# Optimization experiments

Measured on AMD Instinct MI355X. Metric: run time of the kernel, lower is better.

Reference implementation:

```python
import jax, jax.numpy as jnp
import numpy as np

N, D, F, C = 50000, 32, 128, 16
LN_EPS = 1e-5
CLAMP_MIN = 1e-5


def _layernorm_1d(x):
    # LayerNorm over the full node vector, no affine (elementwise_affine=False)
    m = x.mean()
    v = x.var()  # biased, matches torch LayerNorm
    return (x - m) / jnp.sqrt(v + LN_EPS)


def setup_inputs() -> dict:
    key = jax.random.key(0)
    k1, k2, k3, k4, k5, k6 = jax.random.split(key, 6)
    return {
        "h": jax.random.normal(k1, (N, F), dtype=jnp.float32),
        "logits": jax.random.normal(k2, (N, C), dtype=jnp.float32),
        "old_z": jax.random.uniform(k3, (N,), dtype=jnp.float32),
        "tau_1": jax.random.uniform(k4, (1,), dtype=jnp.float32),
        "tau_2": jax.random.uniform(k5, (1,), dtype=jnp.float32),
        "nbr": jax.random.randint(k6, (N, D), 0, N, dtype=jnp.int32),
    }


def reference(h, logits, old_z, tau_1, tau_2, nbr):
    # --- mailbox pass 1: neighbor logits -> adaptive gating features ---
    pred = jnp.argmax(logits[nbr], axis=2)          # [N, D] neighbor class preds
    center_pred = jnp.argmax(logits, axis=1)        # [N]
    # n_degree = 1 in the source (counts, not fractions) -- reproduced faithfully
    f1 = jnp.sum(pred == center_pred[:, None], axis=1).astype(h.dtype)  # [N]
    cnts = jax.nn.one_hot(pred, C, dtype=h.dtype).sum(axis=1)           # [N, C]
    cnts_p = jnp.clip(cnts, CLAMP_MIN, None)
    f2 = -jnp.sum(cnts_p * jnp.log(cnts_p), axis=1)                     # [N]
    f1 = jax.lax.stop_gradient(f1)
    f2 = jax.lax.stop_gradient(f2)

    norm_f1 = _layernorm_1d(f1)
    norm_f2 = _layernorm_1d(f2)
    # shared_tau=True path: tau_1, tau_2 passed in ([1] broadcasts over [N])
    z = jax.nn.sigmoid(-(norm_f1 - tau_1)) * jax.nn.sigmoid(-(norm_f2 - tau_2))  # [N]
    gate = jnp.minimum(old_z, z)

    # --- mailbox pass 2: scatter-sum of neighbor features ---
    agg = h[nbr].sum(axis=1)                        # [N, F]
    normagg = jax.nn.relu(agg)
    new_h = h + gate[:, None] * normagg
    return new_h, z
```

## Files before the change

### kernel.cpp

```cpp
#include <hip/hip_runtime.h>
#include <math.h>

#define NN 50000
#define DEG 32
#define FDIM 128
#define NCLS 16
#define LN_EPS 1e-5f
#define CLAMP_MIN 1e-5f

#define PRED_NB 196
#define CONV_NB 512
#define NGROUPS (NN * FDIM / 8)
#define FEAT_NB 196

#define SLICES 4
#define SL_U32 (NN * 16)
#define AGG_BPS ((NN * 8 + 255) / 256)
#define AGG_NB (SLICES * AGG_BPS)

typedef float  nf4 __attribute__((ext_vector_type(4)));
typedef unsigned nu4 __attribute__((ext_vector_type(4)));
typedef int    ni4 __attribute__((ext_vector_type(4)));

__device__ inline unsigned bf_rne(float x) {
    unsigned u = __float_as_uint(x);
    u += 0x7fffu + ((u >> 16) & 1u);
    return u >> 16;
}

__global__ __launch_bounds__(256) void k_pre(const float* __restrict__ logits,
                                             unsigned char* __restrict__ pred8,
                                             const float* __restrict__ h,
                                             unsigned* __restrict__ hb) {
    int b = blockIdx.x;
    if (b < PRED_NB) {
        int i = b * 256 + threadIdx.x;
        if (i >= NN) return;
        const nf4* lp = (const nf4*)(logits + (long)i * NCLS);
        float best = -INFINITY;
        int bi = 0;
#pragma unroll
        for (int q = 0; q < 4; ++q) {
            nf4 v = __builtin_nontemporal_load(lp + q);
#pragma unroll
            for (int r = 0; r < 4; ++r) {
                if (v[r] > best) { best = v[r]; bi = q * 4 + r; }
            }
        }
        pred8[i] = (unsigned char)bi;
    } else {
        int g0 = (b - PRED_NB) * 256 + threadIdx.x;
        for (int g = g0; g < NGROUPS; g += CONV_NB * 256) {
            const nf4* src = (const nf4*)(h + (long)g * 8);
            nf4 a = __builtin_nontemporal_load(src);
            nf4 c = __builtin_nontemporal_load(src + 1);
            nu4 o;
            o.x = bf_rne(a.x) | (bf_rne(a.y) << 16);
            o.y = bf_rne(a.z) | (bf_rne(a.w) << 16);
            o.z = bf_rne(c.x) | (bf_rne(c.y) << 16);
            o.w = bf_rne(c.z) | (bf_rne(c.w) << 16);
            int node = g >> 4;
            int q    = (g >> 2) & 3;
            int sub  = g & 3;
            ((nu4*)hb)[(size_t)q * (NN * 4) + node * 4 + sub] = o;
        }
    }
}

__global__ __launch_bounds__(256) void k_feats_lds(const int* __restrict__ nbr,
                                                   const unsigned char* __restrict__ pred8,
                                                   float* __restrict__ f1,
                                                   float* __restrict__ f2,
                                                   float* __restrict__ partials, int n) {
    __shared__ unsigned char lp[NN];
    {
        const uint4* s4 = (const uint4*)pred8;
        uint4* d4 = (uint4*)lp;
        for (int i = threadIdx.x; i < 3125; i += 256) d4[i] = s4[i];
    }
    __syncthreads();
    int node = blockIdx.x * 256 + threadIdx.x;
    float v1 = 0.f, v2 = 0.f;
    if (node < n) {
        unsigned long long lo = 0ull, hi = 0ull;
        const int4* np = (const int4*)(nbr + (long)node * DEG);
#pragma unroll
        for (int q = 0; q < 8; ++q) {
            int4 k4 = np[q];
            int ks[4] = {k4.x, k4.y, k4.z, k4.w};
#pragma unroll
            for (int r = 0; r < 4; ++r) {
                int p = lp[ks[r]];
                unsigned long long inc = 1ull << ((p & 7) * 8);
                if (p < 8) lo += inc; else hi += inc;
            }
        }
        int cp = lp[node];
        unsigned long long src = (cp < 8) ? lo : hi;
        v1 = (float)((src >> ((cp & 7) * 8)) & 0xffull);
        float ent = 0.f;
#pragma unroll
        for (int c = 0; c < NCLS; ++c) {
            unsigned long long s = (c < 8) ? lo : hi;
            float cnt = (float)((s >> ((c & 7) * 8)) & 0xffull);
            float x = fmaxf(cnt, CLAMP_MIN);
            ent -= x * logf(x);
        }
        v2 = ent;
        f1[node] = v1;
        f2[node] = v2;
    }
    float s0 = v1, s1 = v1 * v1, s2 = v2, s3 = v2 * v2;
#pragma unroll
    for (int off = 32; off > 0; off >>= 1) {
        s0 += __shfl_down(s0, off);
        s1 += __shfl_down(s1, off);
        s2 += __shfl_down(s2, off);
        s3 += __shfl_down(s3, off);
    }
    __shared__ float red[4][4];
    int wid = threadIdx.x >> 6;
    if ((threadIdx.x & 63) == 0) {
        red[wid][0] = s0; red[wid][1] = s1; red[wid][2] = s2; red[wid][3] = s3;
    }
    __syncthreads();
    if (threadIdx.x == 0) {
        float t0 = 0.f, t1 = 0.f, t2 = 0.f, t3 = 0.f;
#pragma unroll
        for (int w = 0; w < 4; ++w) {
            t0 += red[w][0]; t1 += red[w][1]; t2 += red[w][2]; t3 += red[w][3];
        }
        float* pp = partials + (long)blockIdx.x * 4;
        pp[0] = t0; pp[1] = t1; pp[2] = t2; pp[3] = t3;
    }
}

__global__ __launch_bounds__(256) void k_params(const float* __restrict__ partials,
                                                int nb, float* __restrict__ params) {
    double s0 = 0, s1 = 0, s2 = 0, s3 = 0;
    for (int b = threadIdx.x; b < nb; b += 256) {
        const float* pp = partials + (long)b * 4;
        s0 += (double)pp[0]; s1 += (double)pp[1];
        s2 += (double)pp[2]; s3 += (double)pp[3];
    }
#pragma unroll
    for (int off = 32; off > 0; off >>= 1) {
        s0 += __shfl_down(s0, off);
        s1 += __shfl_down(s1, off);
        s2 += __shfl_down(s2, off);
        s3 += __shfl_down(s3, off);
    }
    __shared__ double red[4][4];
    int wid = threadIdx.x >> 6;
    if ((threadIdx.x & 63) == 0) {
        red[wid][0] = s0; red[wid][1] = s1; red[wid][2] = s2; red[wid][3] = s3;
    }
    __syncthreads();
    if (threadIdx.x == 0) {
        double t0 = 0, t1 = 0, t2 = 0, t3 = 0;
        for (int w = 0; w < 4; ++w) {
            t0 += red[w][0]; t1 += red[w][1]; t2 += red[w][2]; t3 += red[w][3];
        }
        double inv_n = 1.0 / (double)NN;
        double m1 = t0 * inv_n;
        double var1 = t1 * inv_n - m1 * m1;
        double m2 = t2 * inv_n;
        double var2 = t3 * inv_n - m2 * m2;
        params[0] = (float)m1;
        params[1] = (float)(1.0 / sqrt(var1 + (double)LN_EPS));
        params[2] = (float)m2;
        params[3] = (float)(1.0 / sqrt(var2 + (double)LN_EPS));
    }
}

__global__ __launch_bounds__(256) void k_agg_sl(const unsigned* __restrict__ hb,
                                                const int* __restrict__ nbr,
                                                const float* __restrict__ old_z,
                                                const float* __restrict__ tau1,
                                                const float* __restrict__ tau2,
                                                const float* __restrict__ f1,
                                                const float* __restrict__ f2,
                                                const float* __restrict__ params,
                                                float* __restrict__ out_h,
                                                float* __restrict__ out_z, int n) {
    int q = blockIdx.x / AGG_BPS;
    int t = (blockIdx.x - q * AGG_BPS) * 256 + threadIdx.x;
    int node = t >> 3;
    int lane = t & 7;
    if (node >= n) return;
    const unsigned* slab = hb + (size_t)q * SL_U32;
    ni4 k4 = __builtin_nontemporal_load((const ni4*)(nbr + (long)node * DEG) + lane);
    int ks[4] = {k4.x, k4.y, k4.z, k4.w};
    float4 acc = make_float4(0.f, 0.f, 0.f, 0.f);
#pragma unroll
    for (int c = 0; c < 4; ++c) {
        uint2 vs[8];
#pragma unroll
        for (int s = 0; s < 8; ++s) {
            int kj = __shfl(ks[c], s, 8);
            vs[s] = ((const uint2*)(slab + (size_t)kj * 16))[lane];
        }
#pragma unroll
        for (int s = 0; s < 8; ++s) {
            acc.x += __uint_as_float(vs[s].x << 16);
            acc.y += __uint_as_float(vs[s].x & 0xffff0000u);
            acc.z += __uint_as_float(vs[s].y << 16);
            acc.w += __uint_as_float(vs[s].y & 0xffff0000u);
        }
    }
    float a = (f1[node] - params[0]) * params[1] - tau1[0];
    float b = (f2[node] - params[2]) * params[3] - tau2[0];
    float z = 1.f / ((1.f + expf(a)) * (1.f + expf(b)));
    float gate = fminf(old_z[node], z);
    uint2 hid = ((const uint2*)(slab + (size_t)node * 16))[lane];
    nf4 o;
    o.x = __uint_as_float(hid.x << 16)         + gate * fmaxf(acc.x, 0.f);
    o.y = __uint_as_float(hid.x & 0xffff0000u) + gate * fmaxf(acc.y, 0.f);
    o.z = __uint_as_float(hid.y << 16)         + gate * fmaxf(acc.z, 0.f);
    o.w = __uint_as_float(hid.y & 0xffff0000u) + gate * fmaxf(acc.w, 0.f);
    __builtin_nontemporal_store(o, (nf4*)(out_h + (long)node * FDIM + q * 32) + lane);
    if (q == 0 && lane == 0) __builtin_nontemporal_store(z, out_z + node);
}

extern "C" void kernel_launch(void* const* d_in, const int* in_sizes, int n_in,
                              void* d_out, int out_size, void* d_ws, size_t ws_size,
                              hipStream_t stream) {
    const float* h      = (const float*)d_in[0];
    const float* logits = (const float*)d_in[1];
    const float* old_z  = (const float*)d_in[2];
    const float* tau1   = (const float*)d_in[3];
    const float* tau2   = (const float*)d_in[4];
    const int*   nbr    = (const int*)d_in[5];

    char* ws = (char*)d_ws;
    float*         params   = (float*)ws;
    float*         partials = (float*)(ws + 64);
    unsigned char* pred8    = (unsigned char*)(ws + 32768);
    float*         f1       = (float*)(ws + 90112);
    float*         f2       = (float*)(ws + 294912);
    unsigned*      hb       = (unsigned*)(ws + 524288);

    float* out_h = (float*)d_out;
    float* out_z = out_h + (long)NN * FDIM;

    k_pre      <<<PRED_NB + CONV_NB, 256, 0, stream>>>(logits, pred8, h, hb);
    k_feats_lds<<<FEAT_NB, 256, 0, stream>>>(nbr, pred8, f1, f2, partials, NN);
    k_params   <<<1, 256, 0, stream>>>(partials, FEAT_NB, params);
    k_agg_sl   <<<AGG_NB, 256, 0, stream>>>(hb, nbr, old_z, tau1, tau2,
                                            f1, f2, params, out_h, out_z, NN);
}
```

Before: 146.4 us.

## Use 4 lanes per node with 16-byte gathers and double-buffered loads

```diff
diff --git a/kernel.cpp b/kernel.cpp
--- a/kernel.cpp
+++ b/kernel.cpp
@@ -15,7 +15,7 @@
 
 #define SLICES 4
 #define SL_U32 (NN * 16)
-#define AGG_BPS ((NN * 8 + 255) / 256)
+#define AGG_BPS ((NN * 4 + 255) / 256)
 #define AGG_NB (SLICES * AGG_BPS)
 
 typedef float  nf4 __attribute__((ext_vector_type(4)));
@@ -173,6 +173,25 @@
     }
 }
 
+#define U2F(x) __uint_as_float(x)
+
+#define ISSUE(buf, base) do {                                                   \
+    buf[0] = ((const nu4*)(slab + (size_t)kk[(base) + 0] * 16))[lane];          \
+    buf[1] = ((const nu4*)(slab + (size_t)kk[(base) + 1] * 16))[lane];          \
+    buf[2] = ((const nu4*)(slab + (size_t)kk[(base) + 2] * 16))[lane];          \
+    buf[3] = ((const nu4*)(slab + (size_t)kk[(base) + 3] * 16))[lane];          \
+} while (0)
+
+#define CONSUME(buf) do {                                                       \
+    _Pragma("unroll")                                                           \
+    for (int s2 = 0; s2 < 4; ++s2) {                                            \
+        acc[0] += U2F(buf[s2].x << 16); acc[1] += U2F(buf[s2].x & 0xffff0000u); \
+        acc[2] += U2F(buf[s2].y << 16); acc[3] += U2F(buf[s2].y & 0xffff0000u); \
+        acc[4] += U2F(buf[s2].z << 16); acc[5] += U2F(buf[s2].z & 0xffff0000u); \
+        acc[6] += U2F(buf[s2].w << 16); acc[7] += U2F(buf[s2].w & 0xffff0000u); \
+    }                                                                           \
+} while (0)
+
 __global__ __launch_bounds__(256) void k_agg_sl(const unsigned* __restrict__ hb,
                                                 const int* __restrict__ nbr,
                                                 const float* __restrict__ old_z,
@@ -185,40 +204,52 @@
                                                 float* __restrict__ out_z, int n) {
     int q = blockIdx.x / AGG_BPS;
     int t = (blockIdx.x - q * AGG_BPS) * 256 + threadIdx.x;
-    int node = t >> 3;
-    int lane = t & 7;
+    int node = t >> 2;
+    int lane = t & 3;
     if (node >= n) return;
     const unsigned* slab = hb + (size_t)q * SL_U32;
-    ni4 k4 = __builtin_nontemporal_load((const ni4*)(nbr + (long)node * DEG) + lane);
-    int ks[4] = {k4.x, k4.y, k4.z, k4.w};
-    float4 acc = make_float4(0.f, 0.f, 0.f, 0.f);
-#pragma unroll
-    for (int c = 0; c < 4; ++c) {
-        uint2 vs[8];
-#pragma unroll
-        for (int s = 0; s < 8; ++s) {
-            int kj = __shfl(ks[c], s, 8);
-            vs[s] = ((const uint2*)(slab + (size_t)kj * 16))[lane];
-        }
-#pragma unroll
-        for (int s = 0; s < 8; ++s) {
-            acc.x += __uint_as_float(vs[s].x << 16);
-            acc.y += __uint_as_float(vs[s].x & 0xffff0000u);
-            acc.z += __uint_as_float(vs[s].y << 16);
-            acc.w += __uint_as_float(vs[s].y & 0xffff0000u);
-        }
-    }
+
+    const ni4* np = (const ni4*)(nbr + (long)node * DEG);
+    int kk[32];
+#pragma unroll
+    for (int j = 0; j < 8; ++j) {
+        ni4 v = np[j];
+        kk[4 * j + 0] = v.x; kk[4 * j + 1] = v.y;
+        kk[4 * j + 2] = v.z; kk[4 * j + 3] = v.w;
+    }
+
+    float acc[8];
+#pragma unroll
+    for (int i = 0; i < 8; ++i) acc[i] = 0.f;
+
+    nu4 A[4], B[4];
+    ISSUE(A, 0);  ISSUE(B, 4);
+    CONSUME(A);   ISSUE(A, 8);
+    CONSUME(B);   ISSUE(B, 12);
+    CONSUME(A);   ISSUE(A, 16);
+    CONSUME(B);   ISSUE(B, 20);
+    CONSUME(A);   ISSUE(A, 24);
+    CONSUME(B);   ISSUE(B, 28);
+    CONSUME(A);   CONSUME(B);
+
     float a = (f1[node] - params[0]) * params[1] - tau1[0];
     float b = (f2[node] - params[2]) * params[3] - tau2[0];
     float z = 1.f / ((1.f + expf(a)) * (1.f + expf(b)));
     float gate = fminf(old_z[node], z);
-    uint2 hid = ((const uint2*)(slab + (size_t)node * 16))[lane];
-    nf4 o;
-    o.x = __uint_as_float(hid.x << 16)         + gate * fmaxf(acc.x, 0.f);
-    o.y = __uint_as_float(hid.x & 0xffff0000u) + gate * fmaxf(acc.y, 0.f);
-    o.z = __uint_as_float(hid.y << 16)         + gate * fmaxf(acc.z, 0.f);
-    o.w = __uint_as_float(hid.y & 0xffff0000u) + gate * fmaxf(acc.w, 0.f);
-    __builtin_nontemporal_store(o, (nf4*)(out_h + (long)node * FDIM + q * 32) + lane);
+
+    nu4 hid = ((const nu4*)(slab + (size_t)node * 16))[lane];
+    nf4 o0, o1;
+    o0.x = U2F(hid.x << 16)          + gate * fmaxf(acc[0], 0.f);
+    o0.y = U2F(hid.x & 0xffff0000u)  + gate * fmaxf(acc[1], 0.f);
+    o0.z = U2F(hid.y << 16)          + gate * fmaxf(acc[2], 0.f);
+    o0.w = U2F(hid.y & 0xffff0000u)  + gate * fmaxf(acc[3], 0.f);
+    o1.x = U2F(hid.z << 16)          + gate * fmaxf(acc[4], 0.f);
+    o1.y = U2F(hid.z & 0xffff0000u)  + gate * fmaxf(acc[5], 0.f);
+    o1.z = U2F(hid.w << 16)          + gate * fmaxf(acc[6], 0.f);
+    o1.w = U2F(hid.w & 0xffff0000u)  + gate * fmaxf(acc[7], 0.f);
+    nf4* op = (nf4*)(out_h + (long)node * FDIM + q * 32 + lane * 8);
+    __builtin_nontemporal_store(o0, op);
+    __builtin_nontemporal_store(o1, op + 1);
     if (q == 0 && lane == 0) __builtin_nontemporal_store(z, out_z + node);
 }
 
```

Result: no change. 147.7 us (+0.9%).
